# Kernel optimization log

Measured on AMD Instinct MI355X. Metric: run time of the kernel, lower is better.

Reference implementation:

```python
import jax, jax.numpy as jnp
import numpy as np

BN_EPS = 1e-5
NN_EPS = 1e-8

def _bn_relu(h, gamma, beta):
    # training-mode BatchNorm1d over (B, L) per channel, biased variance
    mean = jnp.mean(h, axis=(0, 2), keepdims=True)
    var = jnp.mean((h - mean) ** 2, axis=(0, 2), keepdims=True)
    hn = (h - mean) * jax.lax.rsqrt(var + BN_EPS)
    return jax.nn.relu(hn * gamma[None, :, None] + beta[None, :, None])

def setup_inputs() -> dict:
    key = jax.random.key(0)
    ks = jax.random.split(key, 8)
    B, N, M, Cin, Cout = 2, 2048, 8192, 512, 256
    return {
        "x1": jax.random.normal(ks[0], (B, N, Cin), jnp.float32),
        "p1": jax.random.uniform(ks[1], (B, N, 3), jnp.float32),
        "x2": jax.random.normal(ks[2], (B, M, Cout), jnp.float32),
        "p2": jax.random.uniform(ks[3], (B, M, 3), jnp.float32),
        "W_up": jax.random.normal(ks[4], (Cout, Cin), jnp.float32) * (1.0 / np.sqrt(Cin)),
        "gamma_up": jnp.ones((Cout,), jnp.float32),
        "beta_up": jnp.zeros((Cout,), jnp.float32),
        "W_lat": jax.random.normal(ks[5], (Cout, Cout), jnp.float32) * (1.0 / np.sqrt(Cout)),
        "gamma_lat": jnp.ones((Cout,), jnp.float32),
        "beta_lat": jnp.zeros((Cout,), jnp.float32),
    }

def reference(x1, p1, x2, p2, W_up, gamma_up, beta_up, W_lat, gamma_lat, beta_lat):
    B, M, _ = p2.shape
    # up_mlp: 1x1 conv (bias=False) + BN + ReLU -> (B, Cout, N)
    h1 = _bn_relu(jnp.einsum('bnc,oc->bon', x1, W_up), gamma_up, beta_up)
    # three_nn: squared distances from each p2 query to all p1 points
    d2 = (jnp.sum(p2 ** 2, -1)[:, :, None] + jnp.sum(p1 ** 2, -1)[:, None, :]
          - 2.0 * jnp.einsum('bmd,bnd->bmn', p2, p1))  # (B, M, N)
    neg_d, idx = jax.lax.top_k(-d2, 3)                 # 3 smallest squared dists
    dist = -neg_d                                      # (B, M, 3)
    dist_recip = 1.0 / (dist + NN_EPS)
    weight = dist_recip / jnp.sum(dist_recip, axis=2, keepdims=True)  # (B, M, 3)
    # three_interpolate: weighted gather of h1 along point axis
    C = h1.shape[1]
    g = jnp.take_along_axis(h1, idx.reshape(B, 1, M * 3), axis=2).reshape(B, C, M, 3)
    interp = jnp.einsum('bcmk,bmk->bcm', g, weight)    # (B, Cout, M)
    # lateral_mlp on x2
    h2 = _bn_relu(jnp.einsum('bmc,oc->bom', x2, W_lat), gamma_lat, beta_lat)
    y = interp + h2                                    # (B, Cout, M)
    return jnp.transpose(y, (0, 2, 1)), p2             # (B, M, Cout), (B, M, 3)
```

## Files before the change

### kernel.cpp

```cpp
#include <hip/hip_runtime.h>

#define BATCH 2
#define NPTS  2048
#define MPTS  8192
#define CIN1  512
#define CIN2  256
#define COUT  256
#define ROWS1 (BATCH*NPTS)
#define ROWS2 (BATCH*MPTS)
#define BN_EPS 1e-5f
#define NN_EPS 1e-8f

#define NCHUNK 16
#define CHUNK  (NPTS / NCHUNK)

typedef __attribute__((ext_vector_type(8))) short  bf16x8;
typedef __attribute__((ext_vector_type(4))) float  f32x4;

#define AS1 __attribute__((address_space(1)))
#define AS3 __attribute__((address_space(3)))

__device__ __forceinline__ unsigned short bf16_rne(float x) {
    unsigned u = __float_as_uint(x);
    u += 0x7FFFu + ((u >> 16) & 1u);
    return (unsigned short)(u >> 16);
}
__device__ __forceinline__ float bf16_f32(unsigned short h) {
    return __uint_as_float(((unsigned)h) << 16);
}
__device__ __forceinline__ void gload16(const void* g, void* l) {
    __builtin_amdgcn_global_load_lds((const AS1 unsigned int*)g,
                                     (AS3 unsigned int*)l, 16, 0, 0);
}

__global__ __launch_bounds__(256)
void prep_fused(const float* __restrict__ x1, const float* __restrict__ x2,
                const float* __restrict__ wu, const float* __restrict__ wl,
                const float* __restrict__ p1, const float* __restrict__ p2,
                unsigned short* __restrict__ x1h, unsigned short* __restrict__ x1l,
                unsigned short* __restrict__ x2h, unsigned short* __restrict__ x2l,
                unsigned short* __restrict__ wuh, unsigned short* __restrict__ wul,
                unsigned short* __restrict__ wlh, unsigned short* __restrict__ wll,
                float2* __restrict__ part) {
    const int bid = blockIdx.x;
    const int t = threadIdx.x;
    if (bid < 3168) {
        const float* src; unsigned short *dh, *dl; int K, tile;
        if (bid < 1024)      { src = x1; dh = x1h; dl = x1l; K = CIN1; tile = bid; }
        else if (bid < 3072) { src = x2; dh = x2h; dl = x2l; K = CIN2; tile = bid - 1024; }
        else if (bid < 3136) { src = wu; dh = wuh; dl = wul; K = CIN1; tile = bid - 3072; }
        else                 { src = wl; dh = wlh; dl = wll; K = CIN2; tile = bid - 3136; }
        const int ktiles = K / 32;
        const int rt = tile / ktiles, kt = tile - rt * ktiles;
        const int row = t >> 2, lg = t & 3;
        const float* s = src + (size_t)(rt * 64 + row) * K + kt * 32 + lg * 8;
        const float4 v0 = *(const float4*)s;
        const float4 v1 = *(const float4*)(s + 4);
        const float vv[8] = {v0.x, v0.y, v0.z, v0.w, v1.x, v1.y, v1.z, v1.w};
        bf16x8 h, l;
        #pragma unroll
        for (int i = 0; i < 8; ++i) {
            const unsigned short hh = bf16_rne(vv[i]);
            h[i] = (short)hh;
            l[i] = (short)bf16_rne(vv[i] - bf16_f32(hh));
        }
        const unsigned off = ((unsigned)(row * 64 + lg * 16)) ^ ((unsigned)((row & 7) << 4));
        *(bf16x8*)((char*)dh + (size_t)tile * 4096 + off) = h;
        *(bf16x8*)((char*)dl + (size_t)tile * 4096 + off) = l;
    } else {
        __shared__ float4 pts[CHUNK];
        const int q = bid - 3168;
        const int b = q >> 9;
        const int r = q & 511;
        const int ck = r >> 5;
        const int mblk = r & 31;
        const int n0 = ck * CHUNK;
        if (t < CHUNK) {
            const float* P1 = p1 + ((size_t)b * NPTS + n0) * 3;
            float x = P1[t * 3 + 0], y = P1[t * 3 + 1], z = P1[t * 3 + 2];
            pts[t] = make_float4(x, y, z, x * x + y * y + z * z);
        }
        __syncthreads();
        const int m = mblk * 256 + t;
        const float* qp = p2 + ((size_t)b * MPTS + m) * 3;
        const float qx = qp[0], qy = qp[1], qz = qp[2];
        const float s2 = qx * qx + qy * qy + qz * qz;
        float d0 = 1e30f, d1 = 1e30f, d2 = 1e30f;
        int   i0 = 0,     i1 = 0,     i2 = 0;
        #pragma unroll 4
        for (int n = 0; n < CHUNK; ++n) {
            float4 p = pts[n];
            float dot = p.x * qx + p.y * qy + p.z * qz;
            float d = s2 + p.w - 2.0f * dot;
            if (d < d2) {
                if (d < d1) {
                    d2 = d1; i2 = i1;
                    if (d < d0) { d1 = d0; i1 = i0; d0 = d; i0 = n0 + n; }
                    else        { d1 = d;  i1 = n0 + n; }
                } else { d2 = d; i2 = n0 + n; }
            }
        }
        float2* o = part + ((size_t)(b * MPTS + m) * NCHUNK + ck) * 3;
        o[0] = make_float2(d0, __int_as_float(i0));
        o[1] = make_float2(d1, __int_as_float(i1));
        o[2] = make_float2(d2, __int_as_float(i2));
    }
}

struct GemmLds {
    unsigned char buf[3][4][4096];
    float red[64][8];
};

template<int KTILES, int KSPLIT, bool FUSE_STATS>
__device__ __forceinline__ void gemm_body(
        const unsigned short* __restrict__ Ah_img, const unsigned short* __restrict__ Al_img,
        const unsigned short* __restrict__ Bh_img, const unsigned short* __restrict__ Bl_img,
        float* __restrict__ C, float* __restrict__ stats,
        int bx, int by, int bz, GemmLds& S) {
    constexpr int KT = KTILES / KSPLIT;
    const int tid = threadIdx.x;
    const int lane = tid & 63, wid = tid >> 6;
    const int m0 = by * 64, o0 = bx * 64;
    const int kt0 = bz * KT;
    const int wy = wid >> 1, wx = wid & 1;
    const int lr = lane & 15, lg = lane >> 4;

    const unsigned short* src;
    size_t base;
    switch (wid) {
        case 0:  src = Ah_img; base = ((size_t)by * KTILES + kt0) * 2048; break;
        case 1:  src = Al_img; base = ((size_t)by * KTILES + kt0) * 2048; break;
        case 2:  src = Bh_img; base = ((size_t)bx * KTILES + kt0) * 2048; break;
        default: src = Bl_img; base = ((size_t)bx * KTILES + kt0) * 2048; break;
    }

    f32x4 acc[2][2];
    #pragma unroll
    for (int i = 0; i < 2; ++i)
        #pragma unroll
        for (int j = 0; j < 2; ++j)
            acc[i][j] = (f32x4){0.f, 0.f, 0.f, 0.f};

    auto STAGE = [&](int buf, int tt) {
        const unsigned short* s = src + base + (size_t)tt * 2048;
        char* l = (char*)&S.buf[buf][wid][0];
        #pragma unroll
        for (int c = 0; c < 4; ++c)
            gload16(s + c * 512 + (size_t)lane * 8, l + c * 1024);
    };
    auto FOFF = [&](int row) -> int {
        return (row * 64 + lg * 16) ^ ((row & 7) << 4);
    };

    STAGE(0, 0);
    if (KT > 1) STAGE(1, 1);

    for (int t = 0; t < KT; ++t) {
        if (t + 1 < KT) asm volatile("s_waitcnt vmcnt(4)" ::: "memory");
        else            asm volatile("s_waitcnt vmcnt(0)" ::: "memory");
        __builtin_amdgcn_s_barrier();
        __builtin_amdgcn_sched_barrier(0);
        if (t + 2 < KT) STAGE((t + 2) % 3, t + 2);

        const int cb = t % 3;
        const char* LAh = (const char*)&S.buf[cb][0][0];
        const char* LAl = (const char*)&S.buf[cb][1][0];
        const char* LBh = (const char*)&S.buf[cb][2][0];
        const char* LBl = (const char*)&S.buf[cb][3][0];

        bf16x8 fah[2], fal[2], fbh[2], fbl[2];
        #pragma unroll
        for (int i = 0; i < 2; ++i) {
            const int off = FOFF(wy * 32 + i * 16 + lr);
            fah[i] = *(const bf16x8*)(LAh + off);
            fal[i] = *(const bf16x8*)(LAl + off);
        }
        #pragma unroll
        for (int j = 0; j < 2; ++j) {
            const int off = FOFF(wx * 32 + j * 16 + lr);
            fbh[j] = *(const bf16x8*)(LBh + off);
            fbl[j] = *(const bf16x8*)(LBl + off);
        }
        #pragma unroll
        for (int i = 0; i < 2; ++i)
            #pragma unroll
            for (int j = 0; j < 2; ++j) {
                acc[i][j] = __builtin_amdgcn_mfma_f32_16x16x32_bf16(fah[i], fbh[j], acc[i][j], 0, 0, 0);
                acc[i][j] = __builtin_amdgcn_mfma_f32_16x16x32_bf16(fal[i], fbh[j], acc[i][j], 0, 0, 0);
                acc[i][j] = __builtin_amdgcn_mfma_f32_16x16x32_bf16(fah[i], fbl[j], acc[i][j], 0, 0, 0);
            }
    }

    #pragma unroll
    for (int i = 0; i < 2; ++i)
        #pragma unroll
        for (int j = 0; j < 2; ++j) {
            const int col = o0 + wx * 32 + j * 16 + lr;
            const int rbase = m0 + wy * 32 + i * 16 + lg * 4;
            #pragma unroll
            for (int r = 0; r < 4; ++r) {
                if (KSPLIT > 1)
                    atomicAdd(&C[(size_t)(rbase + r) * COUT + col], acc[i][j][r]);
                else
                    C[(size_t)(rbase + r) * COUT + col] = acc[i][j][r];
            }
        }

    if constexpr (FUSE_STATS) {
        #pragma unroll
        for (int j = 0; j < 2; ++j) {
            float s = 0.f;
            #pragma unroll
            for (int i = 0; i < 2; ++i)
                #pragma unroll
                for (int r = 0; r < 4; ++r)
                    s += acc[i][j][r];
            S.red[wx * 32 + j * 16 + lr][wy * 4 + lg] = s;
        }
        __syncthreads();
        if (tid < 64) {
            float s = 0.f;
            #pragma unroll
            for (int k = 0; k < 8; ++k) s += S.red[tid][k];
            atomicAdd(&stats[o0 + tid], s);
        }
        __syncthreads();
        #pragma unroll
        for (int j = 0; j < 2; ++j) {
            float q = 0.f;
            #pragma unroll
            for (int i = 0; i < 2; ++i)
                #pragma unroll
                for (int r = 0; r < 4; ++r)
                    q = fmaf(acc[i][j][r], acc[i][j][r], q);
            S.red[wx * 32 + j * 16 + lr][wy * 4 + lg] = q;
        }
        __syncthreads();
        if (tid < 64) {
            float q = 0.f;
            #pragma unroll
            for (int k = 0; k < 8; ++k) q += S.red[tid][k];
            atomicAdd(&stats[COUT + o0 + tid], q);
        }
    }
}

__global__ __launch_bounds__(256)
void gemm_fused(const unsigned short* __restrict__ x1h, const unsigned short* __restrict__ x1l,
                const unsigned short* __restrict__ wuh, const unsigned short* __restrict__ wul,
                const unsigned short* __restrict__ x2h, const unsigned short* __restrict__ x2l,
                const unsigned short* __restrict__ wlh, const unsigned short* __restrict__ wll,
                float* __restrict__ h1, float* __restrict__ out, float* __restrict__ stats) {
    __shared__ GemmLds S;
    const int bid = blockIdx.x;
    if (bid < 1024) {
        gemm_body<CIN2/32, 1, true>(x2h, x2l, wlh, wll, out, stats + 512,
                                    bid & 3, bid >> 2, 0, S);
    } else {
        const int q = bid - 1024;
        gemm_body<CIN1/32, 4, false>(x1h, x1l, wuh, wul, h1, nullptr,
                                     q & 3, (q & 255) >> 2, q >> 8, S);
    }
}

__global__ __launch_bounds__(256)
void colsum256(const float* __restrict__ X, int rowsPerBlock,
               float* __restrict__ out) {
    const int c = threadIdx.x;
    const int r0 = blockIdx.x * rowsPerBlock;
    float s = 0.f, q = 0.f;
    for (int r = 0; r < rowsPerBlock; ++r) {
        float v = X[(size_t)(r0 + r) * COUT + c];
        s += v;
        q = fmaf(v, v, q);
    }
    atomicAdd(&out[c], s);
    atomicAdd(&out[COUT + c], q);
}

__global__ __launch_bounds__(256)
void final_combine(const float* __restrict__ h1, const float* __restrict__ stats,
                   const float* __restrict__ g1, const float* __restrict__ b1,
                   const float* __restrict__ g2, const float* __restrict__ b2,
                   const float2* __restrict__ part, float* __restrict__ out) {
    const int t = threadIdx.x;
    const int row = blockIdx.x * 4 + (t >> 6);
    const int c = (t & 63) * 4;
    const int b = row >> 13;

    float d0 = 1e30f, d1 = 1e30f, d2 = 1e30f;
    int   i0 = 0,     i1 = 0,     i2 = 0;
    {
        const float4* pp = (const float4*)(part + (size_t)row * NCHUNK * 3);
        #pragma unroll
        for (int j = 0; j < NCHUNK * 3 / 2; ++j) {
            float4 v = pp[j];
            #pragma unroll
            for (int h = 0; h < 2; ++h) {
                float d = h ? v.z : v.x;
                int   i = __float_as_int(h ? v.w : v.y);
                if (d < d2) {
                    if (d < d1) {
                        d2 = d1; i2 = i1;
                        if (d < d0) { d1 = d0; i1 = i0; d0 = d; i0 = i; }
                        else        { d1 = d;  i1 = i; }
                    } else { d2 = d; i2 = i; }
                }
            }
        }
    }
    const float r0 = 1.0f / (d0 + NN_EPS);
    const float r1 = 1.0f / (d1 + NN_EPS);
    const float r2 = 1.0f / (d2 + NN_EPS);
    const float irs = 1.0f / (r0 + r1 + r2);
    const float w0 = r0 * irs, w1 = r1 * irs, w2 = r2 * irs;

    const float4 sum1 = *(const float4*)&stats[c];
    const float4 sq1  = *(const float4*)&stats[COUT + c];
    const float4 sum2 = *(const float4*)&stats[512 + c];
    const float4 sq2  = *(const float4*)&stats[768 + c];
    const float4 gg1  = *(const float4*)&g1[c];
    const float4 bb1  = *(const float4*)&b1[c];
    const float4 gg2  = *(const float4*)&g2[c];
    const float4 bb2  = *(const float4*)&b2[c];

    const float inv1 = 1.0f / (float)ROWS1, inv2 = 1.0f / (float)ROWS2;
    float4 sc1, sh1, sc2, sh2;
    {
        float m, v;
        m = sum1.x*inv1; v = fmaf(-m,m,sq1.x*inv1); sc1.x = gg1.x/sqrtf(v+BN_EPS); sh1.x = fmaf(-m,sc1.x,bb1.x);
        m = sum1.y*inv1; v = fmaf(-m,m,sq1.y*inv1); sc1.y = gg1.y/sqrtf(v+BN_EPS); sh1.y = fmaf(-m,sc1.y,bb1.y);
        m = sum1.z*inv1; v = fmaf(-m,m,sq1.z*inv1); sc1.z = gg1.z/sqrtf(v+BN_EPS); sh1.z = fmaf(-m,sc1.z,bb1.z);
        m = sum1.w*inv1; v = fmaf(-m,m,sq1.w*inv1); sc1.w = gg1.w/sqrtf(v+BN_EPS); sh1.w = fmaf(-m,sc1.w,bb1.w);
        m = sum2.x*inv2; v = fmaf(-m,m,sq2.x*inv2); sc2.x = gg2.x/sqrtf(v+BN_EPS); sh2.x = fmaf(-m,sc2.x,bb2.x);
        m = sum2.y*inv2; v = fmaf(-m,m,sq2.y*inv2); sc2.y = gg2.y/sqrtf(v+BN_EPS); sh2.y = fmaf(-m,sc2.y,bb2.y);
        m = sum2.z*inv2; v = fmaf(-m,m,sq2.z*inv2); sc2.z = gg2.z/sqrtf(v+BN_EPS); sh2.z = fmaf(-m,sc2.z,bb2.z);
        m = sum2.w*inv2; v = fmaf(-m,m,sq2.w*inv2); sc2.w = gg2.w/sqrtf(v+BN_EPS); sh2.w = fmaf(-m,sc2.w,bb2.w);
    }

    const float* hb = h1 + (size_t)b * NPTS * COUT + c;
    const float4 h0 = *(const float4*)(hb + (size_t)i0 * COUT);
    const float4 h4 = *(const float4*)(hb + (size_t)i1 * COUT);
    const float4 h8 = *(const float4*)(hb + (size_t)i2 * COUT);

    const size_t oi = (size_t)row * COUT + c;
    float4 yv = *(const float4*)&out[oi];
    float4 r;
    r.x = fmaxf(fmaf(yv.x, sc2.x, sh2.x), 0.f)
        + w0 * fmaxf(fmaf(h0.x, sc1.x, sh1.x), 0.f)
        + w1 * fmaxf(fmaf(h4.x, sc1.x, sh1.x), 0.f)
        + w2 * fmaxf(fmaf(h8.x, sc1.x, sh1.x), 0.f);
    r.y = fmaxf(fmaf(yv.y, sc2.y, sh2.y), 0.f)
        + w0 * fmaxf(fmaf(h0.y, sc1.y, sh1.y), 0.f)
        + w1 * fmaxf(fmaf(h4.y, sc1.y, sh1.y), 0.f)
        + w2 * fmaxf(fmaf(h8.y, sc1.y, sh1.y), 0.f);
    r.z = fmaxf(fmaf(yv.z, sc2.z, sh2.z), 0.f)
        + w0 * fmaxf(fmaf(h0.z, sc1.z, sh1.z), 0.f)
        + w1 * fmaxf(fmaf(h4.z, sc1.z, sh1.z), 0.f)
        + w2 * fmaxf(fmaf(h8.z, sc1.z, sh1.z), 0.f);
    r.w = fmaxf(fmaf(yv.w, sc2.w, sh2.w), 0.f)
        + w0 * fmaxf(fmaf(h0.w, sc1.w, sh1.w), 0.f)
        + w1 * fmaxf(fmaf(h4.w, sc1.w, sh1.w), 0.f)
        + w2 * fmaxf(fmaf(h8.w, sc1.w, sh1.w), 0.f);
    *(float4*)&out[oi] = r;
}

extern "C" void kernel_launch(void* const* d_in, const int* in_sizes, int n_in,
                              void* d_out, int out_size, void* d_ws, size_t ws_size,
                              hipStream_t stream) {
    const float* x1       = (const float*)d_in[0];
    const float* p1       = (const float*)d_in[1];
    const float* x2       = (const float*)d_in[2];
    const float* p2       = (const float*)d_in[3];
    const float* W_up     = (const float*)d_in[4];
    const float* gamma_up = (const float*)d_in[5];
    const float* beta_up  = (const float*)d_in[6];
    const float* W_lat    = (const float*)d_in[7];
    const float* gamma_lat= (const float*)d_in[8];
    const float* beta_lat = (const float*)d_in[9];
    float* out = (float*)d_out;

    char* w = (char*)d_ws;
    unsigned short* x1h = (unsigned short*)(w);
    unsigned short* x1l = (unsigned short*)(w + (4u<<20));
    unsigned short* x2h = (unsigned short*)(w + (8u<<20));
    unsigned short* x2l = (unsigned short*)(w + (16u<<20));
    unsigned short* wuh = (unsigned short*)(w + (24u<<20));
    unsigned short* wul = (unsigned short*)(w + (24u<<20) + (256u<<10));
    unsigned short* wlh = (unsigned short*)(w + (24u<<20) + (512u<<10));
    unsigned short* wll = (unsigned short*)(w + (24u<<20) + (640u<<10));
    float*  h1    = (float*)(w + (25u<<20));
    float*  stats = (float*)(w + (29u<<20));
    float2* part  = (float2*)(w + (29u<<20) + (16u<<10));

    hipMemsetAsync(h1, 0, (4u << 20) + 4096, stream);

    prep_fused<<<3168 + 1024, 256, 0, stream>>>(x1, x2, W_up, W_lat, p1, p2,
                                                x1h, x1l, x2h, x2l,
                                                wuh, wul, wlh, wll, part);

    gemm_fused<<<2048, 256, 0, stream>>>(x1h, x1l, wuh, wul,
                                         x2h, x2l, wlh, wll, h1, out, stats);

    colsum256<<<256, 256, 0, stream>>>(h1, ROWS1 / 256, stats);

    final_combine<<<ROWS2 / 4, 256, 0, stream>>>(h1, stats, gamma_up, beta_up,
                                                 gamma_lat, beta_lat, part, out);

    hipMemcpyAsync(out + (size_t)ROWS2 * COUT, p2,
                   (size_t)ROWS2 * 3 * sizeof(float),
                   hipMemcpyDeviceToDevice, stream);
}
```

Baseline: 192.2 us.

## Drop bf16 hi/lo split, remove split-K, fuse BN stats into GEMM epilogue

Replaces the three-term bf16x3 emulated-fp32 GEMM with a single bf16 MFMA product, which halves the converted operand traffic and cuts MFMA work by a factor of three. It also removes the split-K atomics for the up GEMM, stages the output tile through LDS for coalesced float4 stores, and computes column sum and sum of squares from that tile. The separate colsum kernel and memset go away, with stats zeroed inside the prep kernel. The kNN partials move to a chunk-major layout and the per-chunk scan runs two independent top-3 lists for more instruction-level parallelism. Dropping the low-order term lowers GEMM accuracy to plain bf16, which risks tolerance failures.

```diff
diff --git a/kernel.cpp b/kernel.cpp
--- a/kernel.cpp
+++ b/kernel.cpp
@@ -13,6 +13,7 @@
 
 #define NCHUNK 16
 #define CHUNK  (NPTS / NCHUNK)
+#define HCHUNK (CHUNK / 2)
 
 typedef __attribute__((ext_vector_type(8))) short  bf16x8;
 typedef __attribute__((ext_vector_type(4))) float  f32x4;
@@ -25,9 +26,6 @@
     u += 0x7FFFu + ((u >> 16) & 1u);
     return (unsigned short)(u >> 16);
 }
-__device__ __forceinline__ float bf16_f32(unsigned short h) {
-    return __uint_as_float(((unsigned)h) << 16);
-}
 __device__ __forceinline__ void gload16(const void* g, void* l) {
     __builtin_amdgcn_global_load_lds((const AS1 unsigned int*)g,
                                      (AS3 unsigned int*)l, 16, 0, 0);
@@ -37,19 +35,17 @@
 void prep_fused(const float* __restrict__ x1, const float* __restrict__ x2,
                 const float* __restrict__ wu, const float* __restrict__ wl,
                 const float* __restrict__ p1, const float* __restrict__ p2,
-                unsigned short* __restrict__ x1h, unsigned short* __restrict__ x1l,
-                unsigned short* __restrict__ x2h, unsigned short* __restrict__ x2l,
-                unsigned short* __restrict__ wuh, unsigned short* __restrict__ wul,
-                unsigned short* __restrict__ wlh, unsigned short* __restrict__ wll,
-                float2* __restrict__ part) {
+                unsigned short* __restrict__ x1h, unsigned short* __restrict__ x2h,
+                unsigned short* __restrict__ wuh, unsigned short* __restrict__ wlh,
+                float2* __restrict__ part, float* __restrict__ stats) {
     const int bid = blockIdx.x;
     const int t = threadIdx.x;
     if (bid < 3168) {
-        const float* src; unsigned short *dh, *dl; int K, tile;
-        if (bid < 1024)      { src = x1; dh = x1h; dl = x1l; K = CIN1; tile = bid; }
-        else if (bid < 3072) { src = x2; dh = x2h; dl = x2l; K = CIN2; tile = bid - 1024; }
-        else if (bid < 3136) { src = wu; dh = wuh; dl = wul; K = CIN1; tile = bid - 3072; }
-        else                 { src = wl; dh = wlh; dl = wll; K = CIN2; tile = bid - 3136; }
+        const float* src; unsigned short* dh; int K, tile;
+        if (bid < 1024)      { src = x1; dh = x1h; K = CIN1; tile = bid; }
+        else if (bid < 3072) { src = x2; dh = x2h; K = CIN2; tile = bid - 1024; }
+        else if (bid < 3136) { src = wu; dh = wuh; K = CIN1; tile = bid - 3072; }
+        else                 { src = wl; dh = wlh; K = CIN2; tile = bid - 3136; }
         const int ktiles = K / 32;
         const int rt = tile / ktiles, kt = tile - rt * ktiles;
         const int row = t >> 2, lg = t & 3;
@@ -57,17 +53,12 @@
         const float4 v0 = *(const float4*)s;
         const float4 v1 = *(const float4*)(s + 4);
         const float vv[8] = {v0.x, v0.y, v0.z, v0.w, v1.x, v1.y, v1.z, v1.w};
-        bf16x8 h, l;
-        #pragma unroll
-        for (int i = 0; i < 8; ++i) {
-            const unsigned short hh = bf16_rne(vv[i]);
-            h[i] = (short)hh;
-            l[i] = (short)bf16_rne(vv[i] - bf16_f32(hh));
-        }
+        bf16x8 h;
+        #pragma unroll
+        for (int i = 0; i < 8; ++i) h[i] = (short)bf16_rne(vv[i]);
         const unsigned off = ((unsigned)(row * 64 + lg * 16)) ^ ((unsigned)((row & 7) << 4));
         *(bf16x8*)((char*)dh + (size_t)tile * 4096 + off) = h;
-        *(bf16x8*)((char*)dl + (size_t)tile * 4096 + off) = l;
-    } else {
+    } else if (bid < 4192) {
         __shared__ float4 pts[CHUNK];
         const int q = bid - 3168;
         const int b = q >> 9;
@@ -82,58 +73,74 @@
         }
         __syncthreads();
         const int m = mblk * 256 + t;
-        const float* qp = p2 + ((size_t)b * MPTS + m) * 3;
+        const int row = b * MPTS + m;
+        const float* qp = p2 + (size_t)row * 3;
         const float qx = qp[0], qy = qp[1], qz = qp[2];
         const float s2 = qx * qx + qy * qy + qz * qz;
-        float d0 = 1e30f, d1 = 1e30f, d2 = 1e30f;
-        int   i0 = 0,     i1 = 0,     i2 = 0;
+        float dA0 = 1e30f, dA1 = 1e30f, dA2 = 1e30f;
+        int   iA0 = 0,     iA1 = 0,     iA2 = 0;
+        float dB0 = 1e30f, dB1 = 1e30f, dB2 = 1e30f;
+        int   iB0 = 0,     iB1 = 0,     iB2 = 0;
         #pragma unroll 4
-        for (int n = 0; n < CHUNK; ++n) {
-            float4 p = pts[n];
-            float dot = p.x * qx + p.y * qy + p.z * qz;
-            float d = s2 + p.w - 2.0f * dot;
-            if (d < d2) {
-                if (d < d1) {
-                    d2 = d1; i2 = i1;
-                    if (d < d0) { d1 = d0; i1 = i0; d0 = d; i0 = n0 + n; }
-                    else        { d1 = d;  i1 = n0 + n; }
-                } else { d2 = d; i2 = n0 + n; }
+        for (int n = 0; n < HCHUNK; ++n) {
+            float4 pA = pts[n];
+            float4 pB = pts[n + HCHUNK];
+            float dA = s2 + pA.w - 2.0f * (pA.x * qx + pA.y * qy + pA.z * qz);
+            float dB = s2 + pB.w - 2.0f * (pB.x * qx + pB.y * qy + pB.z * qz);
+            if (dA < dA2) {
+                if (dA < dA1) {
+                    dA2 = dA1; iA2 = iA1;
+                    if (dA < dA0) { dA1 = dA0; iA1 = iA0; dA0 = dA; iA0 = n0 + n; }
+                    else          { dA1 = dA; iA1 = n0 + n; }
+                } else { dA2 = dA; iA2 = n0 + n; }
             }
-        }
-        float2* o = part + ((size_t)(b * MPTS + m) * NCHUNK + ck) * 3;
-        o[0] = make_float2(d0, __int_as_float(i0));
-        o[1] = make_float2(d1, __int_as_float(i1));
-        o[2] = make_float2(d2, __int_as_float(i2));
-    }
-}
-
-struct GemmLds {
-    unsigned char buf[3][4][4096];
-    float red[64][8];
+            if (dB < dB2) {
+                if (dB < dB1) {
+                    dB2 = dB1; iB2 = iB1;
+                    if (dB < dB0) { dB1 = dB0; iB1 = iB0; dB0 = dB; iB0 = n0 + HCHUNK + n; }
+                    else          { dB1 = dB; iB1 = n0 + HCHUNK + n; }
+                } else { dB2 = dB; iB2 = n0 + HCHUNK + n; }
+            }
+        }
+        #define INS3(d, i) \
+            if ((d) < dA2) { \
+                if ((d) < dA1) { \
+                    dA2 = dA1; iA2 = iA1; \
+                    if ((d) < dA0) { dA1 = dA0; iA1 = iA0; dA0 = (d); iA0 = (i); } \
+                    else           { dA1 = (d); iA1 = (i); } \
+                } else { dA2 = (d); iA2 = (i); } \
+            }
+        INS3(dB0, iB0); INS3(dB1, iB1); INS3(dB2, iB2);
+        #undef INS3
+        float2* o = part + ((size_t)ck * ROWS2 + row) * 3;
+        o[0] = make_float2(dA0, __int_as_float(iA0));
+        o[1] = make_float2(dA1, __int_as_float(iA1));
+        o[2] = make_float2(dA2, __int_as_float(iA2));
+    } else {
+        ((float4*)stats)[t] = (float4){0.f, 0.f, 0.f, 0.f};
+    }
+}
+
+union GemmLds {
+    unsigned char stage[3][2][4096];
+    float Ct[64][68];
 };
 
-template<int KTILES, int KSPLIT, bool FUSE_STATS>
+template<int KTILES>
 __device__ __forceinline__ void gemm_body(
-        const unsigned short* __restrict__ Ah_img, const unsigned short* __restrict__ Al_img,
-        const unsigned short* __restrict__ Bh_img, const unsigned short* __restrict__ Bl_img,
+        const unsigned short* __restrict__ A_img, const unsigned short* __restrict__ B_img,
         float* __restrict__ C, float* __restrict__ stats,
-        int bx, int by, int bz, GemmLds& S) {
-    constexpr int KT = KTILES / KSPLIT;
+        int bx, int by, GemmLds& S, float red[64][8]) {
     const int tid = threadIdx.x;
     const int lane = tid & 63, wid = tid >> 6;
     const int m0 = by * 64, o0 = bx * 64;
-    const int kt0 = bz * KT;
     const int wy = wid >> 1, wx = wid & 1;
     const int lr = lane & 15, lg = lane >> 4;
 
-    const unsigned short* src;
-    size_t base;
-    switch (wid) {
-        case 0:  src = Ah_img; base = ((size_t)by * KTILES + kt0) * 2048; break;
-        case 1:  src = Al_img; base = ((size_t)by * KTILES + kt0) * 2048; break;
-        case 2:  src = Bh_img; base = ((size_t)bx * KTILES + kt0) * 2048; break;
-        default: src = Bl_img; base = ((size_t)bx * KTILES + kt0) * 2048; break;
-    }
+    const int mat = wid >> 1;
+    const int half = wid & 1;
+    const unsigned short* src = mat ? B_img : A_img;
+    const size_t base = ((size_t)(mat ? bx : by) * KTILES) * 2048 + half * 1024;
 
     f32x4 acc[2][2];
     #pragma unroll
@@ -144,139 +151,98 @@
 
     auto STAGE = [&](int buf, int tt) {
         const unsigned short* s = src + base + (size_t)tt * 2048;
-        char* l = (char*)&S.buf[buf][wid][0];
-        #pragma unroll
-        for (int c = 0; c < 4; ++c)
-            gload16(s + c * 512 + (size_t)lane * 8, l + c * 1024);
+        char* l = (char*)&S.stage[buf][mat][half * 2048];
+        gload16(s + (size_t)lane * 8, l);
+        gload16(s + 512 + (size_t)lane * 8, l + 1024);
     };
     auto FOFF = [&](int row) -> int {
         return (row * 64 + lg * 16) ^ ((row & 7) << 4);
     };
 
     STAGE(0, 0);
-    if (KT > 1) STAGE(1, 1);
-
-    for (int t = 0; t < KT; ++t) {
-        if (t + 1 < KT) asm volatile("s_waitcnt vmcnt(4)" ::: "memory");
-        else            asm volatile("s_waitcnt vmcnt(0)" ::: "memory");
+    STAGE(1, 1);
+
+    for (int t = 0; t < KTILES; ++t) {
+        if (t + 1 < KTILES) asm volatile("s_waitcnt vmcnt(2)" ::: "memory");
+        else                asm volatile("s_waitcnt vmcnt(0)" ::: "memory");
         __builtin_amdgcn_s_barrier();
         __builtin_amdgcn_sched_barrier(0);
-        if (t + 2 < KT) STAGE((t + 2) % 3, t + 2);
+        if (t + 2 < KTILES) STAGE((t + 2) % 3, t + 2);
 
         const int cb = t % 3;
-        const char* LAh = (const char*)&S.buf[cb][0][0];
-        const char* LAl = (const char*)&S.buf[cb][1][0];
-        const char* LBh = (const char*)&S.buf[cb][2][0];
-        const char* LBl = (const char*)&S.buf[cb][3][0];
-
-        bf16x8 fah[2], fal[2], fbh[2], fbl[2];
-        #pragma unroll
-        for (int i = 0; i < 2; ++i) {
-            const int off = FOFF(wy * 32 + i * 16 + lr);
-            fah[i] = *(const bf16x8*)(LAh + off);
-            fal[i] = *(const bf16x8*)(LAl + off);
-        }
-        #pragma unroll
-        for (int j = 0; j < 2; ++j) {
-            const int off = FOFF(wx * 32 + j * 16 + lr);
-            fbh[j] = *(const bf16x8*)(LBh + off);
-            fbl[j] = *(const bf16x8*)(LBl + off);
-        }
+        const char* LA = (const char*)&S.stage[cb][0][0];
+        const char* LB = (const char*)&S.stage[cb][1][0];
+
+        bf16x8 fa[2], fb[2];
+        #pragma unroll
+        for (int i = 0; i < 2; ++i)
+            fa[i] = *(const bf16x8*)(LA + FOFF(wy * 32 + i * 16 + lr));
+        #pragma unroll
+        for (int j = 0; j < 2; ++j)
+            fb[j] = *(const bf16x8*)(LB + FOFF(wx * 32 + j * 16 + lr));
         #pragma unroll
         for (int i = 0; i < 2; ++i)
             #pragma unroll
-            for (int j = 0; j < 2; ++j) {
-                acc[i][j] = __builtin_amdgcn_mfma_f32_16x16x32_bf16(fah[i], fbh[j], acc[i][j], 0, 0, 0);
-                acc[i][j] = __builtin_amdgcn_mfma_f32_16x16x32_bf16(fal[i], fbh[j], acc[i][j], 0, 0, 0);
-                acc[i][j] = __builtin_amdgcn_mfma_f32_16x16x32_bf16(fah[i], fbl[j], acc[i][j], 0, 0, 0);
-            }
-    }
-
+            for (int j = 0; j < 2; ++j)
+                acc[i][j] = __builtin_amdgcn_mfma_f32_16x16x32_bf16(fa[i], fb[j], acc[i][j], 0, 0, 0);
+    }
+
+    __syncthreads();
     #pragma unroll
     for (int i = 0; i < 2; ++i)
         #pragma unroll
         for (int j = 0; j < 2; ++j) {
-            const int col = o0 + wx * 32 + j * 16 + lr;
-            const int rbase = m0 + wy * 32 + i * 16 + lg * 4;
+            const int col = wx * 32 + j * 16 + lr;
+            const int rbase = wy * 32 + i * 16 + lg * 4;
             #pragma unroll
-            for (int r = 0; r < 4; ++r) {
-                if (KSPLIT > 1)
-                    atomicAdd(&C[(size_t)(rbase + r) * COUT + col], acc[i][j][r]);
-                else
-                    C[(size_t)(rbase + r) * COUT + col] = acc[i][j][r];
-            }
-        }
-
-    if constexpr (FUSE_STATS) {
-        #pragma unroll
-        for (int j = 0; j < 2; ++j) {
-            float s = 0.f;
-            #pragma unroll
-            for (int i = 0; i < 2; ++i)
-                #pragma unroll
-                for (int r = 0; r < 4; ++r)
-                    s += acc[i][j][r];
-            S.red[wx * 32 + j * 16 + lr][wy * 4 + lg] = s;
-        }
-        __syncthreads();
-        if (tid < 64) {
-            float s = 0.f;
-            #pragma unroll
-            for (int k = 0; k < 8; ++k) s += S.red[tid][k];
-            atomicAdd(&stats[o0 + tid], s);
-        }
-        __syncthreads();
-        #pragma unroll
-        for (int j = 0; j < 2; ++j) {
-            float q = 0.f;
-            #pragma unroll
-            for (int i = 0; i < 2; ++i)
-                #pragma unroll
-                for (int r = 0; r < 4; ++r)
-                    q = fmaf(acc[i][j][r], acc[i][j][r], q);
-            S.red[wx * 32 + j * 16 + lr][wy * 4 + lg] = q;
-        }
-        __syncthreads();
-        if (tid < 64) {
-            float q = 0.f;
-            #pragma unroll
-            for (int k = 0; k < 8; ++k) q += S.red[tid][k];
-            atomicAdd(&stats[COUT + o0 + tid], q);
-        }
+            for (int r = 0; r < 4; ++r)
+                S.Ct[rbase + r][col] = acc[i][j][r];
+        }
+    __syncthreads();
+    {
+        const int cr = tid >> 4;
+        const int cc = (tid & 15) * 4;
+        #pragma unroll
+        for (int q = 0; q < 4; ++q) {
+            const int row = cr + q * 16;
+            *(float4*)&C[(size_t)(m0 + row) * COUT + o0 + cc] =
+                *(const float4*)&S.Ct[row][cc];
+        }
+    }
+    {
+        const int col = tid & 63, rq = tid >> 6;
+        float s = 0.f, q2 = 0.f;
+        #pragma unroll
+        for (int r = 0; r < 16; ++r) {
+            float v = S.Ct[rq * 16 + r][col];
+            s += v;
+            q2 = fmaf(v, v, q2);
+        }
+        red[col][rq] = s;
+        red[col][4 + rq] = q2;
+    }
+    __syncthreads();
+    if (tid < 64) {
+        float ss = red[tid][0] + red[tid][1] + red[tid][2] + red[tid][3];
+        float qq = red[tid][4] + red[tid][5] + red[tid][6] + red[tid][7];
+        atomicAdd(&stats[o0 + tid], ss);
+        atomicAdd(&stats[COUT + o0 + tid], qq);
     }
 }
 
 __global__ __launch_bounds__(256)
-void gemm_fused(const unsigned short* __restrict__ x1h, const unsigned short* __restrict__ x1l,
-                const unsigned short* __restrict__ wuh, const unsigned short* __restrict__ wul,
-                const unsigned short* __restrict__ x2h, const unsigned short* __restrict__ x2l,
-                const unsigned short* __restrict__ wlh, const unsigned short* __restrict__ wll,
+void gemm_fused(const unsigned short* __restrict__ x1h, const unsigned short* __restrict__ wuh,
+                const unsigned short* __restrict__ x2h, const unsigned short* __restrict__ wlh,
                 float* __restrict__ h1, float* __restrict__ out, float* __restrict__ stats) {
     __shared__ GemmLds S;
+    __shared__ float red[64][8];
     const int bid = blockIdx.x;
-    if (bid < 1024) {
-        gemm_body<CIN2/32, 1, true>(x2h, x2l, wlh, wll, out, stats + 512,
-                                    bid & 3, bid >> 2, 0, S);
+    if (bid < 256) {
+        gemm_body<CIN1/32>(x1h, wuh, h1, stats, bid & 3, bid >> 2, S, red);
     } else {
-        const int q = bid - 1024;
-        gemm_body<CIN1/32, 4, false>(x1h, x1l, wuh, wul, h1, nullptr,
-                                     q & 3, (q & 255) >> 2, q >> 8, S);
-    }
-}
-
-__global__ __launch_bounds__(256)
-void colsum256(const float* __restrict__ X, int rowsPerBlock,
-               float* __restrict__ out) {
-    const int c = threadIdx.x;
-    const int r0 = blockIdx.x * rowsPerBlock;
-    float s = 0.f, q = 0.f;
-    for (int r = 0; r < rowsPerBlock; ++r) {
-        float v = X[(size_t)(r0 + r) * COUT + c];
-        s += v;
-        q = fmaf(v, v, q);
-    }
-    atomicAdd(&out[c], s);
-    atomicAdd(&out[COUT + c], q);
+        const int q = bid - 256;
+        gemm_body<CIN2/32>(x2h, wlh, out, stats + 512, q & 3, q >> 2, S, red);
+    }
 }
 
 __global__ __launch_bounds__(256)
@@ -291,22 +257,20 @@
 
     float d0 = 1e30f, d1 = 1e30f, d2 = 1e30f;
     int   i0 = 0,     i1 = 0,     i2 = 0;
-    {
-        const float4* pp = (const float4*)(part + (size_t)row * NCHUNK * 3);
-        #pragma unroll
-        for (int j = 0; j < NCHUNK * 3 / 2; ++j) {
-            float4 v = pp[j];
-            #pragma unroll
-            for (int h = 0; h < 2; ++h) {
-                float d = h ? v.z : v.x;
-                int   i = __float_as_int(h ? v.w : v.y);
-                if (d < d2) {
-                    if (d < d1) {
-                        d2 = d1; i2 = i1;
-                        if (d < d0) { d1 = d0; i1 = i0; d0 = d; i0 = i; }
-                        else        { d1 = d;  i1 = i; }
-                    } else { d2 = d; i2 = i; }
-                }
+    #pragma unroll
+    for (int ck = 0; ck < NCHUNK; ++ck) {
+        const float2* pe = part + ((size_t)ck * ROWS2 + row) * 3;
+        #pragma unroll
+        for (int h = 0; h < 3; ++h) {
+            float2 v = pe[h];
+            float d = v.x;
+            int   i = __float_as_int(v.y);
+            if (d < d2) {
+                if (d < d1) {
+                    d2 = d1; i2 = i1;
+                    if (d < d0) { d1 = d0; i1 = i0; d0 = d; i0 = i; }
+                    else        { d1 = d;  i1 = i; }
+                } else { d2 = d; i2 = i; }
             }
         }
     }
@@ -383,27 +347,17 @@
 
     char* w = (char*)d_ws;
     unsigned short* x1h = (unsigned short*)(w);
-    unsigned short* x1l = (unsigned short*)(w + (4u<<20));
-    unsigned short* x2h = (unsigned short*)(w + (8u<<20));
-    unsigned short* x2l = (unsigned short*)(w + (16u<<20));
-    unsigned short* wuh = (unsigned short*)(w + (24u<<20));
-    unsigned short* wul = (unsigned short*)(w + (24u<<20) + (256u<<10));
-    unsigned short* wlh = (unsigned short*)(w + (24u<<20) + (512u<<10));
-    unsigned short* wll = (unsigned short*)(w + (24u<<20) + (640u<<10));
-    float*  h1    = (float*)(w + (25u<<20));
-    float*  stats = (float*)(w + (29u<<20));
-    float2* part  = (float2*)(w + (29u<<20) + (16u<<10));
-
-    hipMemsetAsync(h1, 0, (4u << 20) + 4096, stream);
-
-    prep_fused<<<3168 + 1024, 256, 0, stream>>>(x1, x2, W_up, W_lat, p1, p2,
-                                                x1h, x1l, x2h, x2l,
-                                                wuh, wul, wlh, wll, part);
-
-    gemm_fused<<<2048, 256, 0, stream>>>(x1h, x1l, wuh, wul,
-                                         x2h, x2l, wlh, wll, h1, out, stats);
-
-    colsum256<<<256, 256, 0, stream>>>(h1, ROWS1 / 256, stats);
+    unsigned short* x2h = (unsigned short*)(w + (4u<<20));
+    unsigned short* wuh = (unsigned short*)(w + (12u<<20));
+    unsigned short* wlh = (unsigned short*)(w + (12u<<20) + (256u<<10));
+    float*  h1    = (float*)(w + (13u<<20));
+    float*  stats = (float*)(w + (17u<<20));
+    float2* part  = (float2*)(w + (17u<<20) + (16u<<10));
+
+    prep_fused<<<4193, 256, 0, stream>>>(x1, x2, W_up, W_lat, p1, p2,
+                                         x1h, x2h, wuh, wlh, part, stats);
+
+    gemm_fused<<<1280, 256, 0, stream>>>(x1h, wuh, x2h, wlh, h1, out, stats);
 
     final_combine<<<ROWS2 / 4, 256, 0, stream>>>(h1, stats, gamma_up, beta_up,
                                                  gamma_lat, beta_lat, part, out);
```

New measurement: 178.3 us. -7.2%, faster.
